# Optimization experiments

Measured on AMD Instinct MI355X. Metric: run time of the kernel, lower is better.

## Reference

```python
import jax, jax.numpy as jnp
import numpy as np

B, J, O = 32, 20, 20
D, H, F, L = 256, 8, 1024, 6
S = J * O
DH = D // H
NL = L + 1  # 6 encoder blocks + final block stacked together


def setup_inputs() -> dict:
    ks = jax.random.split(jax.random.key(0), 16)
    s = 0.02
    am = jax.random.randint(ks[4], (B, J), 0, 2) == 1
    am = am.at[:, 0].set(False)  # at least one unmasked job per row (avoid all -inf softmax)
    return {
        "operations": jax.random.normal(ks[0], (B, J, O, 2), jnp.float32),
        "job_ops_mask": jax.random.normal(ks[1], (B, J, O, O), jnp.float32),
        "ops_machines_mask": jax.random.normal(ks[2], (B, S, S), jnp.float32),
        "jobs_next_op_idx": jax.random.randint(ks[3], (B, J, 1), 0, O),
        "action_mask": am,
        "qkv_w": jax.random.normal(ks[5], (NL, 3 * D, D), jnp.float32) * s,
        "qkv_b": jnp.zeros((NL, 3 * D), jnp.float32),
        "out_w": jax.random.normal(ks[6], (NL, D, D), jnp.float32) * s,
        "out_b": jnp.zeros((NL, D), jnp.float32),
        "ln1_g": jnp.ones((NL, D), jnp.float32),
        "ln1_b": jnp.zeros((NL, D), jnp.float32),
        "ln2_g": jnp.ones((NL, D), jnp.float32),
        "ln2_b": jnp.zeros((NL, D), jnp.float32),
        "ff1_w": jax.random.normal(ks[7], (NL, F, D), jnp.float32) * s,
        "ff1_b": jnp.zeros((NL, F), jnp.float32),
        "ff2_w": jax.random.normal(ks[8], (NL, D, F), jnp.float32) * s,
        "ff2_b": jnp.zeros((NL, D), jnp.float32),
        "op_emb_w": jax.random.normal(ks[9], (D, 2), jnp.float32) * s,
        "op_emb_b": jnp.zeros((D,), jnp.float32),
        "pol_w": jax.random.normal(ks[10], (1, D), jnp.float32) * s,
        "pol_b": jnp.zeros((1,), jnp.float32),
    }


def _ln(x, g, b):
    m = x.mean(-1, keepdims=True)
    v = ((x - m) ** 2).mean(-1, keepdims=True)
    return (x - m) * jax.lax.rsqrt(v + 1e-5) * g + b


def _mha(x, mask, qw, qb, ow, ob):
    N, Sq, _ = x.shape
    qkv = x @ qw.T + qb
    q, k, v = jnp.split(qkv, 3, axis=-1)
    q = q.reshape(N, Sq, H, DH).transpose(0, 2, 1, 3)
    k = k.reshape(N, Sq, H, DH).transpose(0, 2, 1, 3)
    v = v.reshape(N, Sq, H, DH).transpose(0, 2, 1, 3)
    sc = jnp.einsum("nhqd,nhkd->nhqk", q, k) / jnp.sqrt(jnp.float32(DH))
    sc = sc + mask  # additive float attn mask, broadcast over heads where needed
    a = jax.nn.softmax(sc, axis=-1)
    o = jnp.einsum("nhqk,nhkd->nhqd", a, v).transpose(0, 2, 1, 3).reshape(N, Sq, D)
    return o @ ow.T + ob


def _forward(operations, job_ops_mask, ops_machines_mask, jobs_next_op_idx, action_mask,
             qkv_w, qkv_b, out_w, out_b, ln1_g, ln1_b, ln2_g, ln2_b,
             ff1_w, ff1_b, ff2_w, ff2_b, op_emb_w, op_emb_b, pol_w, pol_b):
    def block(x, mask, i):  # pre-norm TransformerEncoderLayer, gelu, dropout=0
        h = _ln(x, ln1_g[i], ln1_b[i])
        x = x + _mha(h, mask, qkv_w[i], qkv_b[i], out_w[i], out_b[i])
        h = _ln(x, ln2_g[i], ln2_b[i])
        ff = jax.nn.gelu(h @ ff1_w[i].T + ff1_b[i], approximate=False) @ ff2_w[i].T + ff2_b[i]
        return x + ff

    # sinusoidal positional encoding over the operation index
    pos = jnp.arange(O, dtype=jnp.float32)[:, None]
    div = jnp.exp(jnp.arange(0, D, 2, dtype=jnp.float32) * (-np.log(10000.0) / D))
    pe = jnp.stack([jnp.sin(pos * div), jnp.cos(pos * div)], axis=-1).reshape(O, D)
    x = operations @ op_emb_w.T + op_emb_b + pe[None, None]  # (B,J,O,D)

    # ALiBi slopes: 1/x^(i+1), x = 256^(1/H)
    base = (2.0 ** 8) ** (1.0 / H)
    slope = (1.0 / base ** jnp.arange(1, H + 1, dtype=jnp.float32))[None, :, None, None]
    job_mask = job_ops_mask.reshape(B * J, 1, O, O) * slope  # (B*J, H, O, O)
    mach_mask = ops_machines_mask[:, None, :, :]  # (B, 1, S, S), identical across heads

    for i in range(L):
        if i % 2 == 0:  # per-job attention over operations
            x = block(x.reshape(B * J, O, D), job_mask, i).reshape(B, J, O, D)
        else:  # per-machine attention over all operations
            x = block(x.reshape(B, S, D), mach_mask, i).reshape(B, J, O, D)

    idx = jnp.broadcast_to(jobs_next_op_idx[:, :, :, None], (B, J, 1, D))
    nxt = jnp.take_along_axis(x, idx, axis=2)[:, :, 0, :]  # (B, J, D)
    kp = jnp.where(action_mask, -jnp.inf, 0.0)[:, None, None, :]  # key padding mask
    nxt = block(nxt, kp, L)
    logits = (nxt @ pol_w.T + pol_b)[:, :, 0]
    return jnp.where(action_mask, -jnp.inf, logits)


def reference(operations, job_ops_mask, ops_machines_mask, jobs_next_op_idx, action_mask,
              qkv_w, qkv_b, out_w, out_b, ln1_g, ln1_b, ln2_g, ln2_b,
              ff1_w, ff1_b, ff2_w, ff2_b, op_emb_w, op_emb_b, pol_w, pol_b):
    return _forward(operations, job_ops_mask, ops_machines_mask, jobs_next_op_idx, action_mask,
                    qkv_w, qkv_b, out_w, out_b, ln1_g, ln1_b, ln2_g, ln2_b,
                    ff1_w, ff1_b, ff2_w, ff2_b, op_emb_w, op_emb_b, pol_w, pol_b)
```

## Files before the change

kernel.cpp:

```cpp
#include <hip/hip_runtime.h>
#include <math.h>

#define B_  32
#define J_  20
#define O_  20
#define S_  400
#define D_  256
#define H_  8
#define F_  1024
#define L_  6
#define T_  12800
#define T2_ 640

#define NEG_BIG (-1e30f)

typedef __attribute__((ext_vector_type(8))) short short8;
typedef __attribute__((ext_vector_type(4))) float f32x4;

__device__ __forceinline__ short f2b(float f) {
  union { float f; unsigned u; } c; c.f = f;
  unsigned r = (c.u + 0x7FFFu + ((c.u >> 16) & 1u)) >> 16;
  return (short)r;
}
__device__ __forceinline__ float b2f(short s) {
  union { unsigned u; float f; } c;
  c.u = ((unsigned)(unsigned short)s) << 16;
  return c.f;
}
__device__ __forceinline__ unsigned addpk(unsigned a, unsigned b) {
  union { unsigned u; float f; } x, y;
  x.u = a << 16;        y.u = b << 16;        float lo = x.f + y.f;
  x.u = a & 0xffff0000u; y.u = b & 0xffff0000u; float hi = x.f + y.f;
  return (unsigned)(unsigned short)f2b(lo) | ((unsigned)(unsigned short)f2b(hi) << 16);
}
__device__ __forceinline__ void async_copy16(const short* g, short* l) {
  __builtin_amdgcn_global_load_lds(
      (const __attribute__((address_space(1))) void*)g,
      (__attribute__((address_space(3))) void*)l, 16, 0, 0);
}

__global__ __launch_bounds__(256) void k_f2b4(
    const float* __restrict__ s0, short* __restrict__ d0,
    const float* __restrict__ s1, short* __restrict__ d1,
    const float* __restrict__ s2, short* __restrict__ d2,
    const float* __restrict__ s3, short* __restrict__ d3)
{
  int bid = blockIdx.x;
  const float* src; short* dst; int base;
  if (bid < 672)        { src = s0; dst = d0; base = bid; }
  else if (bid < 896)   { src = s1; dst = d1; base = bid - 672; }
  else if (bid < 1792)  { src = s2; dst = d2; base = bid - 896; }
  else                  { src = s3; dst = d3; base = bid - 1792; }
  int i = (base * 256 + threadIdx.x) * 8;
  float4 a = *(const float4*)(src + i);
  float4 b = *(const float4*)(src + i + 4);
  short8 o;
  o[0] = f2b(a.x); o[1] = f2b(a.y); o[2] = f2b(a.z); o[3] = f2b(a.w);
  o[4] = f2b(b.x); o[5] = f2b(b.y); o[6] = f2b(b.z); o[7] = f2b(b.w);
  *(short8*)(dst + i) = o;
}

__global__ __launch_bounds__(640) void k_maskconv(
    const void* __restrict__ am_raw, int* __restrict__ am_out)
{
  __shared__ int isInt32;
  const int tid = threadIdx.x;
  if (tid == 0) isInt32 = 1;
  __syncthreads();
  if (tid < 160) {
    int v = ((const int*)am_raw)[tid];
    if (v != 0 && v != 1) atomicAnd(&isInt32, 0);
  }
  __syncthreads();
  if (tid < 640) {
    int v;
    if (isInt32) v = ((const int*)am_raw)[tid] != 0;
    else         v = ((const unsigned char*)am_raw)[tid] != 0;
    am_out[tid] = v;
  }
}

__global__ __launch_bounds__(256) void k_embed(
    const float* __restrict__ ops, const float* __restrict__ ew,
    const float* __restrict__ eb, short* __restrict__ x)
{
  int idx = blockIdx.x * 256 + threadIdx.x;
  int d = idx & 255;
  int t = idx >> 8;
  int o = t % O_;
  float a0 = ops[(size_t)t * 2 + 0], a1 = ops[(size_t)t * 2 + 1];
  int k = d >> 1;
  float div = expf((float)(2 * k) * -0.03597789207803197f);
  float ang = (float)o * div;
  float pe = (d & 1) ? cosf(ang) : sinf(ang);
  x[idx] = f2b(a0 * ew[d * 2 + 0] + a1 * ew[d * 2 + 1] + eb[d] + pe);
}

__global__ __launch_bounds__(256) void k_ln(
    const short* __restrict__ x, const float* __restrict__ g, const float* __restrict__ b,
    short* __restrict__ out, int nTok)
{
  int gid = blockIdx.x * 256 + threadIdx.x;
  int tok = gid >> 6, lane = threadIdx.x & 63;
  if (tok >= nTok) return;
  int2 pk = ((const int2*)(x + (size_t)tok * 256))[lane];
  union { unsigned u; float f; } c;
  float vx, vy, vz, vw;
  c.u = (unsigned)pk.x << 16;        vx = c.f;
  c.u = (unsigned)pk.x & 0xffff0000u; vy = c.f;
  c.u = (unsigned)pk.y << 16;        vz = c.f;
  c.u = (unsigned)pk.y & 0xffff0000u; vw = c.f;
  float s = vx + vy + vz + vw;
  #pragma unroll
  for (int off = 32; off > 0; off >>= 1) s += __shfl_down(s, off);
  float mean = __shfl(s, 0) * (1.f / 256.f);
  float dx = vx - mean, dy = vy - mean, dz = vz - mean, dw = vw - mean;
  float q = dx * dx + dy * dy + dz * dz + dw * dw;
  #pragma unroll
  for (int off = 32; off > 0; off >>= 1) q += __shfl_down(q, off);
  float var = __shfl(q, 0) * (1.f / 256.f);
  float inv = 1.f / sqrtf(var + 1e-5f);
  float4 gv = ((const float4*)g)[lane];
  float4 bv = ((const float4*)b)[lane];
  float ox = dx * inv * gv.x + bv.x;
  float oy = dy * inv * gv.y + bv.y;
  float oz = dz * inv * gv.z + bv.z;
  float ow = dw * inv * gv.w + bv.w;
  int2 po;
  po.x = (int)(unsigned short)f2b(ox) | ((int)(unsigned short)f2b(oy) << 16);
  po.y = (int)(unsigned short)f2b(oz) | ((int)(unsigned short)f2b(ow) << 16);
  ((int2*)(out + (size_t)tok * 256))[lane] = po;
}

__global__ __launch_bounds__(256) void k_gemm_bf16(
    const short* __restrict__ A, const short* __restrict__ W,
    const float* __restrict__ bias, const short* __restrict__ R,
    short* __restrict__ C, int M, int N, int K, int act)
{
  __shared__ short LDS_[17408];
  short* Asf = LDS_;
  short* Bsf = LDS_ + 8192;
  short* Csf = LDS_;
  const int tid  = threadIdx.x;
  const int lane = tid & 63;
  const int wv   = tid >> 6;
  const int lm   = lane & 15;
  const int quad = lane >> 4;
  const int wm   = (wv >> 1) * 64;
  const int wn   = (wv & 1) * 64;
  const int n0 = blockIdx.x * 128;
  const int m0 = blockIdx.y * 128;

  f32x4 acc[4][4] = {};

  for (int k0 = 0; k0 < K; k0 += 64) {
    __syncthreads();
    #pragma unroll
    for (int i = 0; i < 4; ++i) {
      const int c    = tid + 256 * i;
      const int row  = c >> 3;
      const int kc8  = ((c & 7) ^ (row & 7)) * 8;
      async_copy16(A + (size_t)(m0 + row) * K + k0 + kc8, &Asf[c * 8]);
      async_copy16(W + (size_t)(n0 + row) * K + k0 + kc8, &Bsf[c * 8]);
    }
    __syncthreads();
    #pragma unroll
    for (int kh = 0; kh < 2; ++kh) {
      short8 af[4], bf[4];
      #pragma unroll
      for (int i = 0; i < 4; ++i) {
        const int row  = wm + i * 16 + lm;
        const int slot = (kh * 4 + quad) ^ (lm & 7);
        af[i] = *(short8*)&Asf[(row * 8 + slot) * 8];
      }
      #pragma unroll
      for (int j = 0; j < 4; ++j) {
        const int row  = wn + j * 16 + lm;
        const int slot = (kh * 4 + quad) ^ (lm & 7);
        bf[j] = *(short8*)&Bsf[(row * 8 + slot) * 8];
      }
      #pragma unroll
      for (int i = 0; i < 4; ++i)
        #pragma unroll
        for (int j = 0; j < 4; ++j)
          acc[i][j] = __builtin_amdgcn_mfma_f32_16x16x32_bf16(af[i], bf[j], acc[i][j], 0, 0, 0);
    }
  }

  __syncthreads();
  #pragma unroll
  for (int j = 0; j < 4; ++j) {
    const int ccol = wn + j * 16 + lm;
    const float bv = bias[n0 + ccol];
    #pragma unroll
    for (int i = 0; i < 4; ++i) {
      #pragma unroll
      for (int r = 0; r < 4; ++r) {
        const int row = wm + i * 16 + quad * 4 + r;
        float vvv = acc[i][j][r] + bv;
        if (act) vvv = vvv / (1.f + __expf(-1.702f * vvv));
        Csf[row * 136 + ccol] = f2b(vvv);
      }
    }
  }
  __syncthreads();
  {
    const int srow = tid >> 1, sh = (tid & 1) * 64;
    const size_t gbase = (size_t)(m0 + srow) * N + n0 + sh;
    const short* ls = &Csf[srow * 136 + sh];
    #pragma unroll
    for (int u = 0; u < 8; ++u) {
      uint4 v = *(const uint4*)(ls + u * 8);
      if (R) {
        uint4 rv = *(const uint4*)(R + gbase + u * 8);
        v.x = addpk(v.x, rv.x); v.y = addpk(v.y, rv.y);
        v.z = addpk(v.z, rv.z); v.w = addpk(v.w, rv.w);
      }
      *(uint4*)(C + gbase + u * 8) = v;
    }
  }
}

__global__ __launch_bounds__(256) void k_gemm_ln(
    const short* __restrict__ A, const short* __restrict__ W,
    const float* __restrict__ bias, const short* __restrict__ R,
    short* __restrict__ X, short* __restrict__ Hout,
    const float* __restrict__ g, const float* __restrict__ bb_,
    int M, int K)
{
  __shared__ short LDS_[4096 + 16896];
  short* Asf = LDS_;
  short* Bsf = LDS_ + 4096;
  short* Csf = LDS_ + 4096;
  const int tid  = threadIdx.x;
  const int lane = tid & 63;
  const int wv   = tid >> 6;
  const int lm   = lane & 15;
  const int quad = lane >> 4;
  const int wn   = wv * 64;
  const int m0   = blockIdx.x * 64;

  f32x4 acc[4][4] = {};

  for (int k0 = 0; k0 < K; k0 += 64) {
    __syncthreads();
    #pragma unroll
    for (int i = 0; i < 2; ++i) {
      const int c   = tid + 256 * i;
      const int row = c >> 3;
      const int kc8 = ((c & 7) ^ (row & 7)) * 8;
      async_copy16(A + (size_t)(m0 + row) * K + k0 + kc8, &Asf[c * 8]);
    }
    #pragma unroll
    for (int i = 0; i < 8; ++i) {
      const int c   = tid + 256 * i;
      const int row = c >> 3;
      const int kc8 = ((c & 7) ^ (row & 7)) * 8;
      async_copy16(W + (size_t)row * K + k0 + kc8, &Bsf[c * 8]);
    }
    __syncthreads();
    #pragma unroll
    for (int kh = 0; kh < 2; ++kh) {
      short8 af[4], bf[4];
      #pragma unroll
      for (int i = 0; i < 4; ++i) {
        const int row  = i * 16 + lm;
        const int slot = (kh * 4 + quad) ^ (lm & 7);
        af[i] = *(short8*)&Asf[(row * 8 + slot) * 8];
      }
      #pragma unroll
      for (int j = 0; j < 4; ++j) {
        const int row  = wn + j * 16 + lm;
        const int slot = (kh * 4 + quad) ^ (lm & 7);
        bf[j] = *(short8*)&Bsf[(row * 8 + slot) * 8];
      }
      #pragma unroll
      for (int i = 0; i < 4; ++i)
        #pragma unroll
        for (int j = 0; j < 4; ++j)
          acc[i][j] = __builtin_amdgcn_mfma_f32_16x16x32_bf16(af[i], bf[j], acc[i][j], 0, 0, 0);
    }
  }

  __syncthreads();
  #pragma unroll
  for (int j = 0; j < 4; ++j) {
    const int ccol = wn + j * 16 + lm;
    const float bv = bias[ccol];
    #pragma unroll
    for (int i = 0; i < 4; ++i) {
      #pragma unroll
      for (int r = 0; r < 4; ++r) {
        const int row = i * 16 + quad * 4 + r;
        Csf[row * 264 + ccol] = f2b(acc[i][j][r] + bv);
      }
    }
  }
  __syncthreads();

  {
    const int row = tid >> 2, cb = (tid & 3) * 64;
    const size_t gbase = (size_t)(m0 + row) * 256 + cb;
    const short* ls = &Csf[row * 264 + cb];
    uint4 xv[8];
    float s1 = 0.f, s2 = 0.f;
    #pragma unroll
    for (int u = 0; u < 8; ++u) {
      uint4 v = *(const uint4*)(ls + u * 8);
      uint4 rv = *(const uint4*)(R + gbase + u * 8);
      v.x = addpk(v.x, rv.x); v.y = addpk(v.y, rv.y);
      v.z = addpk(v.z, rv.z); v.w = addpk(v.w, rv.w);
      xv[u] = v;
      *(uint4*)(X + gbase + u * 8) = v;
      #pragma unroll
      for (int w2 = 0; w2 < 4; ++w2) {
        unsigned pv = (&v.x)[w2];
        union { unsigned u; float f; } c1, c2;
        c1.u = pv << 16; c2.u = pv & 0xffff0000u;
        s1 += c1.f + c2.f;
        s2 += c1.f * c1.f + c2.f * c2.f;
      }
    }
    s1 += __shfl_xor(s1, 1); s2 += __shfl_xor(s2, 1);
    s1 += __shfl_xor(s1, 2); s2 += __shfl_xor(s2, 2);
    const float mean = s1 * (1.f / 256.f);
    const float var  = s2 * (1.f / 256.f) - mean * mean;
    const float inv  = 1.f / sqrtf(var + 1e-5f);
    #pragma unroll
    for (int u = 0; u < 8; ++u) {
      float4 g0 = *(const float4*)(g + cb + u * 8);
      float4 g1 = *(const float4*)(g + cb + u * 8 + 4);
      float4 b0 = *(const float4*)(bb_ + cb + u * 8);
      float4 b1 = *(const float4*)(bb_ + cb + u * 8 + 4);
      auto lnpk = [&](unsigned pv, float ga, float gb2, float ba, float bb2) -> unsigned {
        union { unsigned u; float f; } c1, c2;
        c1.u = pv << 16; c2.u = pv & 0xffff0000u;
        float lo = (c1.f - mean) * inv * ga + ba;
        float hi = (c2.f - mean) * inv * gb2 + bb2;
        return (unsigned)(unsigned short)f2b(lo) | ((unsigned)(unsigned short)f2b(hi) << 16);
      };
      uint4 hv;
      hv.x = lnpk(xv[u].x, g0.x, g0.y, b0.x, b0.y);
      hv.y = lnpk(xv[u].y, g0.z, g0.w, b0.z, b0.w);
      hv.z = lnpk(xv[u].z, g1.x, g1.y, b1.x, b1.y);
      hv.w = lnpk(xv[u].w, g1.z, g1.w, b1.z, b1.w);
      *(uint4*)(Hout + gbase + u * 8) = hv;
    }
  }
}

#define QSTR 776
#define PSTR20 40
__global__ __launch_bounds__(512) void k_attn20_mfma(
    const short* __restrict__ qkv, short* __restrict__ att,
    const float* __restrict__ jmask, const int* __restrict__ amask, int mode)
{
  __shared__ short QK[32 * QSTR];
  __shared__ short Ps[8][32 * PSTR20];
  const int seq  = blockIdx.x;
  const int tid  = threadIdx.x;
  const int wv   = tid >> 6;
  const int lane = tid & 63;
  const int l15  = lane & 15;
  const int quad = lane >> 4;
  const float scale = 0.1767766952966369f;

  for (int e = tid; e < 3072; e += 512) {
    int row = e / 96, c8 = (e % 96) * 8;
    uint4 v = {0u, 0u, 0u, 0u};
    if (row < 20) v = *(const uint4*)(qkv + ((size_t)seq * 20 + row) * 768 + c8);
    *(uint4*)&QK[row * QSTR + c8] = v;
  }
  __syncthreads();

  const short8 aq0 = *(short8*)&QK[(0  + l15) * QSTR + wv * 32 + quad * 8];
  const short8 aq1 = *(short8*)&QK[(16 + l15) * QSTR + wv * 32 + quad * 8];
  const short8 bk0 = *(short8*)&QK[(0  + l15) * QSTR + 256 + wv * 32 + quad * 8];
  const short8 bk1 = *(short8*)&QK[(16 + l15) * QSTR + 256 + wv * 32 + quad * 8];
  f32x4 z4 = {0.f, 0.f, 0.f, 0.f};
  f32x4 s00 = __builtin_amdgcn_mfma_f32_16x16x32_bf16(aq0, bk0, z4, 0, 0, 0);
  f32x4 s01 = __builtin_amdgcn_mfma_f32_16x16x32_bf16(aq0, bk1, z4, 0, 0, 0);
  f32x4 s10 = __builtin_amdgcn_mfma_f32_16x16x32_bf16(aq1, bk0, z4, 0, 0, 0);
  f32x4 s11 = __builtin_amdgcn_mfma_f32_16x16x32_bf16(aq1, bk1, z4, 0, 0, 0);

  const float slope = exp2f(-(float)(wv + 1));
  short* psw = &Ps[wv][0];
  float l0[4] = {0.f, 0.f, 0.f, 0.f};
  float l1[4] = {0.f, 0.f, 0.f, 0.f};

  #pragma unroll
  for (int kt = 0; kt < 2; ++kt) {
    const int k  = kt * 16 + l15;
    const int kc = (k < 20) ? k : 19;
    float madd1 = 0.f;
    if (mode == 1) madd1 = amask[seq * 20 + kc] ? NEG_BIG : 0.f;
    #pragma unroll
    for (int qt = 0; qt < 2; ++qt) {
      f32x4 s = (kt == 0) ? (qt == 0 ? s00 : s10) : (qt == 0 ? s01 : s11);
      #pragma unroll
      for (int r = 0; r < 4; ++r) {
        const int q  = qt * 16 + quad * 4 + r;
        const int qc = (q < 20) ? q : 19;
        float sv = s[r] * scale;
        if (mode == 0) sv += jmask[(size_t)seq * 400 + qc * 20 + kc] * slope;
        else           sv += madd1;
        float p = (k < 20) ? __expf(fminf(sv, 40.f)) : 0.f;
        if (qt == 0) l0[r] += p; else l1[r] += p;
        psw[q * PSTR20 + k] = f2b(p);
      }
    }
  }
  #pragma unroll
  for (int r = 0; r < 4; ++r) {
    float t0 = l0[r];
    t0 += __shfl_xor(t0, 1); t0 += __shfl_xor(t0, 2);
    t0 += __shfl_xor(t0, 4); t0 += __shfl_xor(t0, 8);
    l0[r] = 1.f / t0;
    float t1 = l1[r];
    t1 += __shfl_xor(t1, 1); t1 += __shfl_xor(t1, 2);
    t1 += __shfl_xor(t1, 4); t1 += __shfl_xor(t1, 8);
    l1[r] = 1.f / t1;
  }

  const short8 pf0 = *(short8*)&psw[(0  + l15) * PSTR20 + quad * 8];
  const short8 pf1 = *(short8*)&psw[(16 + l15) * PSTR20 + quad * 8];
  #pragma unroll
  for (int dt = 0; dt < 2; ++dt) {
    const int d = wv * 32 + dt * 16 + l15;
    short8 vf;
    #pragma unroll
    for (int j = 0; j < 8; ++j)
      vf[j] = QK[(quad * 8 + j) * QSTR + 512 + d];
    f32x4 o0 = __builtin_amdgcn_mfma_f32_16x16x32_bf16(pf0, vf, z4, 0, 0, 0);
    f32x4 o1 = __builtin_amdgcn_mfma_f32_16x16x32_bf16(pf1, vf, z4, 0, 0, 0);
    #pragma unroll
    for (int r = 0; r < 4; ++r) {
      const int q = quad * 4 + r;
      att[((size_t)seq * 20 + q) * 256 + d] = f2b(o0[r] * l0[r]);
    }
    if (quad == 0) {
      #pragma unroll
      for (int r = 0; r < 4; ++r) {
        const int q = 16 + r;
        att[((size_t)seq * 20 + q) * 256 + d] = f2b(o1[r] * l1[r]);
      }
    }
  }
}

#define VSTR 36
#define PSTRW 40
__global__ __launch_bounds__(512) void k_attn400_mfma(
    const short* __restrict__ qkv, short* __restrict__ att,
    const float* __restrict__ mmask)
{
  __shared__ short Wl[8 * 1792];

  const int id   = blockIdx.x;
  const int b    = (id >> 3) / 25 * 8 + (id & 7);
  const int qt   = (id >> 3) % 25;
  const int tid  = threadIdx.x;
  const int wv   = tid >> 6;
  const int lane = tid & 63;
  const int l15  = lane & 15;
  const int quad = lane >> 4;
  const int q0   = qt * 16;
  const float scale = 0.1767766952966369f;

  short* Vw = &Wl[wv * 1792];
  short* Pw = &Wl[wv * 1792 + 1152];
  const short* qbase = qkv + (size_t)b * 400 * 768;

  const short8 af = *(const short8*)(qbase + (size_t)(q0 + l15) * 768 + wv * 32 + quad * 8);

  f32x4 accO[2] = {};
  float lsum = 0.f;
  const float* mrow = mmask + ((size_t)b * 400 + q0 + l15) * 400;

  const int vrow = lane >> 1;
  const int vch  = (lane & 1) * 2;
  const int vdst = vrow * VSTR + vch * 8;

  short8 kf0, kf1;
  float4 mA4, mB4;
  auto prefKM = [&](int k0) {
    kf0 = *(const short8*)(qbase + (size_t)(k0 + l15) * 768 + 256 + wv * 32 + quad * 8);
    int kr = k0 + 16 + l15; if (kr > 399) kr = 399;
    kf1 = *(const short8*)(qbase + (size_t)kr * 768 + 256 + wv * 32 + quad * 8);
    mA4 = *(const float4*)(mrow + k0 + quad * 4);
    int kb = k0 + 16 + quad * 4; if (kb > 396) kb = 396;
    mB4 = *(const float4*)(mrow + kb);
  };
  prefKM(0);

  for (int k0 = 0; k0 < 416; k0 += 32) {
    int vr = k0 + vrow; if (vr > 399) vr = 399;
    const short* vp = qbase + (size_t)vr * 768 + 512 + wv * 32 + vch * 8;
    const uint4 v0 = *(const uint4*)vp;
    const uint4 v1 = *(const uint4*)(vp + 8);

    const short8 ck0 = kf0, ck1 = kf1;
    const float4 cA = mA4, cB = mB4;

    f32x4 z4 = {0.f, 0.f, 0.f, 0.f};
    f32x4 s0 = __builtin_amdgcn_mfma_f32_16x16x32_bf16(ck0, af, z4, 0, 0, 0);
    f32x4 s1 = __builtin_amdgcn_mfma_f32_16x16x32_bf16(ck1, af, z4, 0, 0, 0);

    if (k0 + 32 < 416) prefKM(k0 + 32);

    float p0[4], p1[4];
    #pragma unroll
    for (int r = 0; r < 4; ++r) {
      const int kB = k0 + 16 + quad * 4 + r;
      float svA = s0[r] * scale + (&cA.x)[r];
      float svB = (kB < 400) ? (s1[r] * scale + (&cB.x)[r]) : NEG_BIG;
      p0[r] = __expf(fminf(svA, 40.f));
      p1[r] = __expf(fminf(svB, 40.f));
      lsum += p0[r] + p1[r];
    }

    unsigned pk00, pk01, pk10, pk11;
    asm("v_cvt_pk_bf16_f32 %0, %1, %2" : "=v"(pk00) : "v"(p0[0]), "v"(p0[1]));
    asm("v_cvt_pk_bf16_f32 %0, %1, %2" : "=v"(pk01) : "v"(p0[2]), "v"(p0[3]));
    asm("v_cvt_pk_bf16_f32 %0, %1, %2" : "=v"(pk10) : "v"(p1[0]), "v"(p1[1]));
    asm("v_cvt_pk_bf16_f32 %0, %1, %2" : "=v"(pk11) : "v"(p1[2]), "v"(p1[3]));
    uint2 w0; w0.x = pk00; w0.y = pk01;
    uint2 w1; w1.x = pk10; w1.y = pk11;
    *(uint2*)&Pw[l15 * PSTRW + quad * 4]      = w0;
    *(uint2*)&Pw[l15 * PSTRW + 16 + quad * 4] = w1;
    const short8 pf = *(short8*)&Pw[l15 * PSTRW + quad * 8];

    *(uint4*)&Vw[vdst]     = v0;
    *(uint4*)&Vw[vdst + 8] = v1;
    #pragma unroll
    for (int c = 0; c < 2; ++c) {
      short8 vf;
      #pragma unroll
      for (int j = 0; j < 8; ++j)
        vf[j] = Vw[(quad * 8 + j) * VSTR + c * 16 + l15];
      accO[c] = __builtin_amdgcn_mfma_f32_16x16x32_bf16(vf, pf, accO[c], 0, 0, 0);
    }
  }

  lsum += __shfl_xor(lsum, 16);
  lsum += __shfl_xor(lsum, 32);
  const float inv = 1.f / lsum;

  #pragma unroll
  for (int c = 0; c < 2; ++c) {
    float a0 = accO[c][0] * inv, a1 = accO[c][1] * inv;
    float a2 = accO[c][2] * inv, a3 = accO[c][3] * inv;
    unsigned o01, o23;
    asm("v_cvt_pk_bf16_f32 %0, %1, %2" : "=v"(o01) : "v"(a0), "v"(a1));
    asm("v_cvt_pk_bf16_f32 %0, %1, %2" : "=v"(o23) : "v"(a2), "v"(a3));
    uint2 ov; ov.x = o01; ov.y = o23;
    *(uint2*)&att[((size_t)b * 400 + q0 + l15) * 256 + wv * 32 + c * 16 + quad * 4] = ov;
  }
}

__global__ __launch_bounds__(256) void k_gather2(
    const short* __restrict__ x, const short* __restrict__ h,
    const int* __restrict__ idx, short* __restrict__ x2, short* __restrict__ h2)
{
  int t = blockIdx.x * 256 + threadIdx.x;
  if (t >= 640 * 16) return;
  int bj = t >> 4, c = t & 15;
  int o = idx[bj];
  size_t src = ((size_t)bj * 20 + o) * 256;
  ((uint4*)(x2 + (size_t)bj * 256))[c] = ((const uint4*)(x + src))[c];
  ((uint4*)(h2 + (size_t)bj * 256))[c] = ((const uint4*)(h + src))[c];
}

__global__ __launch_bounds__(256) void k_logits(
    const short* __restrict__ x2, const float* __restrict__ pw, const float* __restrict__ pb,
    const int* __restrict__ am, float* __restrict__ out)
{
  int gid = blockIdx.x * 256 + threadIdx.x;
  int row = gid >> 6, lane = threadIdx.x & 63;
  int2 pk = ((const int2*)(x2 + (size_t)row * 256))[lane];
  union { unsigned u; float f; } c;
  float vx, vy, vz, vw;
  c.u = (unsigned)pk.x << 16;         vx = c.f;
  c.u = (unsigned)pk.x & 0xffff0000u; vy = c.f;
  c.u = (unsigned)pk.y << 16;         vz = c.f;
  c.u = (unsigned)pk.y & 0xffff0000u; vw = c.f;
  float4 w = ((const float4*)pw)[lane];
  float s = vx * w.x + vy * w.y + vz * w.z + vw * w.w;
  #pragma unroll
  for (int off = 32; off > 0; off >>= 1) s += __shfl_down(s, off);
  if (lane == 0) out[row] = am[row] ? NEG_BIG : (s + pb[0]);
}

extern "C" void kernel_launch(void* const* d_in, const int* in_sizes, int n_in,
                              void* d_out, int out_size, void* d_ws, size_t ws_size,
                              hipStream_t stream)
{
  (void)in_sizes; (void)n_in; (void)out_size; (void)ws_size;
  const float* operations        = (const float*)d_in[0];
  const float* job_ops_mask      = (const float*)d_in[1];
  const float* ops_machines_mask = (const float*)d_in[2];
  const int*   jobs_next_op_idx  = (const int*)d_in[3];
  const void*  action_mask_raw   = (const void*)d_in[4];
  const float* qkv_w = (const float*)d_in[5];
  const float* qkv_b = (const float*)d_in[6];
  const float* out_w = (const float*)d_in[7];
  const float* out_b = (const float*)d_in[8];
  const float* ln1_g = (const float*)d_in[9];
  const float* ln1_b = (const float*)d_in[10];
  const float* ln2_g = (const float*)d_in[11];
  const float* ln2_b = (const float*)d_in[12];
  const float* ff1_w = (const float*)d_in[13];
  const float* ff1_b = (const float*)d_in[14];
  const float* ff2_w = (const float*)d_in[15];
  const float* ff2_b = (const float*)d_in[16];
  const float* op_emb_w = (const float*)d_in[17];
  const float* op_emb_b = (const float*)d_in[18];
  const float* pol_w = (const float*)d_in[19];
  const float* pol_b = (const float*)d_in[20];
  float* out = (float*)d_out;

  short* x    = (short*)d_ws;
  short* x2   = x + (size_t)T_ * D_;
  short* h    = x2 + (size_t)T2_ * D_;
  short* big  = h + (size_t)T_ * D_;
  short* h2   = big + (size_t)T_ * F_;
  short* big2 = h2 + (size_t)T2_ * D_;
  int*   amc  = (int*)(big2 + (size_t)T2_ * F_);
  short* bwq  = (short*)(amc + 640);
  short* bwo  = bwq + (size_t)7 * 768 * 256;
  short* bwf1 = bwo + (size_t)7 * 256 * 256;
  short* bwf2 = bwf1 + (size_t)7 * 1024 * 256;

  auto gemm = [&](const short* A, const short* Wb, const float* bias, const short* R,
                  short* C, int M, int N, int K, int act) {
    k_gemm_bf16<<<dim3(N / 128, M / 128), dim3(256), 0, stream>>>(
        A, Wb, bias, R, C, M, N, K, act);
  };
  auto gemm_ln = [&](const short* A, const short* Wb, const float* bias, const short* R,
                     short* X, short* Hout, const float* g, const float* b, int M, int K) {
    k_gemm_ln<<<dim3(M / 64), dim3(256), 0, stream>>>(
        A, Wb, bias, R, X, Hout, g, b, M, K);
  };

  k_f2b4<<<dim3(2688), 256, 0, stream>>>(qkv_w, bwq, out_w, bwo, ff1_w, bwf1, ff2_w, bwf2);
  k_maskconv<<<dim3(1), dim3(640), 0, stream>>>(action_mask_raw, amc);
  k_embed<<<dim3(T_ * D_ / 256), dim3(256), 0, stream>>>(operations, op_emb_w, op_emb_b, x);
  k_ln<<<dim3(T_ / 4), 256, 0, stream>>>(x, ln1_g, ln1_b, h, T_);

  for (int i = 0; i < L_; ++i) {
    const short* qw  = bwq  + (size_t)i * 768 * 256;
    const float* qb  = qkv_b + (size_t)i * 768;
    const short* ow  = bwo  + (size_t)i * 256 * 256;
    const float* ob  = out_b + (size_t)i * 256;
    const short* f1w = bwf1 + (size_t)i * 1024 * 256;
    const float* f1b = ff1_b + (size_t)i * 1024;
    const short* f2w = bwf2 + (size_t)i * 256 * 1024;
    const float* f2b_ = ff2_b + (size_t)i * 256;
    gemm(h, qw, qb, nullptr, big, T_, 768, 256, 0);
    if ((i & 1) == 0)
      k_attn20_mfma<<<dim3(640), 512, 0, stream>>>(big, h, job_ops_mask, nullptr, 0);
    else
      k_attn400_mfma<<<dim3(800), 512, 0, stream>>>(big, h, ops_machines_mask);
    gemm_ln(h, ow, ob, x, x, h, ln2_g + i * D_, ln2_b + i * D_, T_, 256);
    gemm(h, f1w, f1b, nullptr, big, T_, 1024, 256, 1);
    gemm_ln(big, f2w, f2b_, x, x, h, ln1_g + (i + 1) * D_, ln1_b + (i + 1) * D_, T_, 1024);
  }

  k_gather2<<<dim3(40), 256, 0, stream>>>(x, h, jobs_next_op_idx, x2, h2);

  {
    int i = L_;
    const short* qw  = bwq  + (size_t)i * 768 * 256;
    const float* qb  = qkv_b + (size_t)i * 768;
    const short* ow  = bwo  + (size_t)i * 256 * 256;
    const float* ob  = out_b + (size_t)i * 256;
    const short* f1w = bwf1 + (size_t)i * 1024 * 256;
    const float* f1b = ff1_b + (size_t)i * 1024;
    const short* f2w = bwf2 + (size_t)i * 256 * 1024;
    const float* f2b_ = ff2_b + (size_t)i * 256;
    gemm(h2, qw, qb, nullptr, big2, T2_, 768, 256, 0);
    k_attn20_mfma<<<dim3(32), 512, 0, stream>>>(big2, h2, nullptr, amc, 1);
    gemm_ln(h2, ow, ob, x2, x2, h2, ln2_g + i * D_, ln2_b + i * D_, T2_, 256);
    gemm(h2, f1w, f1b, nullptr, big2, T2_, 1024, 256, 1);
    gemm(big2, f2w, f2b_, x2, x2, T2_, 256, 1024, 0);
  }

  k_logits<<<dim3(160), 256, 0, stream>>>(x2, pol_w, pol_b, amc, out);
}
```

Before: 982.8 us.

## Convert machine mask to bf16 once and stage per-tile mask rows in LDS

The 400x400 machine attention mask is converted to bf16 once per call in the weight-conversion kernel (2500 extra blocks), so each of the three machine-attention layers reads half the bytes. Each attention block cooperatively loads its 16 mask rows into shared memory, removing per-wave redundant global float4 mask loads (8 waves read the same rows). V loads are also prefetched one iteration ahead and written to LDS earlier. Trade-offs: the mask is rounded to bf16, which changes precision, and there is an extra conversion pass plus extra LDS use.

```diff
diff --git a/kernel.cpp b/kernel.cpp
--- a/kernel.cpp
+++ b/kernel.cpp
@@ -43,14 +43,16 @@
     const float* __restrict__ s0, short* __restrict__ d0,
     const float* __restrict__ s1, short* __restrict__ d1,
     const float* __restrict__ s2, short* __restrict__ d2,
-    const float* __restrict__ s3, short* __restrict__ d3)
+    const float* __restrict__ s3, short* __restrict__ d3,
+    const float* __restrict__ s4, short* __restrict__ d4)
 {
   int bid = blockIdx.x;
   const float* src; short* dst; int base;
   if (bid < 672)        { src = s0; dst = d0; base = bid; }
   else if (bid < 896)   { src = s1; dst = d1; base = bid - 672; }
   else if (bid < 1792)  { src = s2; dst = d2; base = bid - 896; }
-  else                  { src = s3; dst = d3; base = bid - 1792; }
+  else if (bid < 2688)  { src = s3; dst = d3; base = bid - 1792; }
+  else                  { src = s4; dst = d4; base = bid - 2688; }
   int i = (base * 256 + threadIdx.x) * 8;
   float4 a = *(const float4*)(src + i);
   float4 b = *(const float4*)(src + i + 4);
@@ -450,11 +452,13 @@
 
 #define VSTR 36
 #define PSTRW 40
+#define MSTR 424
 __global__ __launch_bounds__(512) void k_attn400_mfma(
     const short* __restrict__ qkv, short* __restrict__ att,
-    const float* __restrict__ mmask)
+    const short* __restrict__ mbf)
 {
   __shared__ short Wl[8 * 1792];
+  __shared__ short Ml[16 * MSTR];
 
   const int id   = blockIdx.x;
   const int b    = (id >> 3) / 25 * 8 + (id & 7);
@@ -467,6 +471,14 @@
   const int q0   = qt * 16;
   const float scale = 0.1767766952966369f;
 
+  for (int e = tid; e < 16 * 52; e += 512) {
+    const int row = e / 52, cc = e % 52;
+    uint4 v = {0u, 0u, 0u, 0u};
+    if (cc < 50)
+      v = *(const uint4*)(mbf + ((size_t)(b * 400 + q0 + row)) * 400 + cc * 8);
+    *(uint4*)&Ml[row * MSTR + cc * 8] = v;
+  }
+
   short* Vw = &Wl[wv * 1792];
   short* Pw = &Wl[wv * 1792 + 1152];
   const short* qbase = qkv + (size_t)b * 400 * 768;
@@ -475,45 +487,65 @@
 
   f32x4 accO[2] = {};
   float lsum = 0.f;
-  const float* mrow = mmask + ((size_t)b * 400 + q0 + l15) * 400;
 
   const int vrow = lane >> 1;
   const int vch  = (lane & 1) * 2;
   const int vdst = vrow * VSTR + vch * 8;
 
   short8 kf0, kf1;
-  float4 mA4, mB4;
-  auto prefKM = [&](int k0) {
+  uint4  nv0, nv1;
+  auto prefK = [&](int k0) {
     kf0 = *(const short8*)(qbase + (size_t)(k0 + l15) * 768 + 256 + wv * 32 + quad * 8);
     int kr = k0 + 16 + l15; if (kr > 399) kr = 399;
     kf1 = *(const short8*)(qbase + (size_t)kr * 768 + 256 + wv * 32 + quad * 8);
-    mA4 = *(const float4*)(mrow + k0 + quad * 4);
-    int kb = k0 + 16 + quad * 4; if (kb > 396) kb = 396;
-    mB4 = *(const float4*)(mrow + kb);
   };
-  prefKM(0);
-
-  for (int k0 = 0; k0 < 416; k0 += 32) {
+  auto prefV = [&](int k0) {
     int vr = k0 + vrow; if (vr > 399) vr = 399;
     const short* vp = qbase + (size_t)vr * 768 + 512 + wv * 32 + vch * 8;
-    const uint4 v0 = *(const uint4*)vp;
-    const uint4 v1 = *(const uint4*)(vp + 8);
-
+    nv0 = *(const uint4*)vp;
+    nv1 = *(const uint4*)(vp + 8);
+  };
+  prefK(0);
+  prefV(0);
+
+  __syncthreads();
+
+  const short* mrow = &Ml[l15 * MSTR];
+
+  for (int k0 = 0; k0 < 416; k0 += 32) {
+    const uint4 v0 = nv0, v1 = nv1;
     const short8 ck0 = kf0, ck1 = kf1;
-    const float4 cA = mA4, cB = mB4;
+
+    *(uint4*)&Vw[vdst]     = v0;
+    *(uint4*)&Vw[vdst + 8] = v1;
 
     f32x4 z4 = {0.f, 0.f, 0.f, 0.f};
     f32x4 s0 = __builtin_amdgcn_mfma_f32_16x16x32_bf16(ck0, af, z4, 0, 0, 0);
     f32x4 s1 = __builtin_amdgcn_mfma_f32_16x16x32_bf16(ck1, af, z4, 0, 0, 0);
 
-    if (k0 + 32 < 416) prefKM(k0 + 32);
+    if (k0 + 32 < 416) { prefK(k0 + 32); prefV(k0 + 32); }
+
+    uint2 ma = *(const uint2*)(mrow + k0 + quad * 4);
+    uint2 mb = *(const uint2*)(mrow + k0 + 16 + quad * 4);
+    float mAv[4], mBv[4];
+    {
+      union { unsigned u; float f; } c;
+      c.u = ma.x << 16;         mAv[0] = c.f;
+      c.u = ma.x & 0xffff0000u; mAv[1] = c.f;
+      c.u = ma.y << 16;         mAv[2] = c.f;
+      c.u = ma.y & 0xffff0000u; mAv[3] = c.f;
+      c.u = mb.x << 16;         mBv[0] = c.f;
+      c.u = mb.x & 0xffff0000u; mBv[1] = c.f;
+      c.u = mb.y << 16;         mBv[2] = c.f;
+      c.u = mb.y & 0xffff0000u; mBv[3] = c.f;
+    }
 
     float p0[4], p1[4];
     #pragma unroll
     for (int r = 0; r < 4; ++r) {
       const int kB = k0 + 16 + quad * 4 + r;
-      float svA = s0[r] * scale + (&cA.x)[r];
-      float svB = (kB < 400) ? (s1[r] * scale + (&cB.x)[r]) : NEG_BIG;
+      float svA = s0[r] * scale + mAv[r];
+      float svB = (kB < 400) ? (s1[r] * scale + mBv[r]) : NEG_BIG;
       p0[r] = __expf(fminf(svA, 40.f));
       p1[r] = __expf(fminf(svB, 40.f));
       lsum += p0[r] + p1[r];
@@ -530,8 +562,6 @@
     *(uint2*)&Pw[l15 * PSTRW + 16 + quad * 4] = w1;
     const short8 pf = *(short8*)&Pw[l15 * PSTRW + quad * 8];
 
-    *(uint4*)&Vw[vdst]     = v0;
-    *(uint4*)&Vw[vdst + 8] = v1;
     #pragma unroll
     for (int c = 0; c < 2; ++c) {
       short8 vf;
@@ -630,6 +660,7 @@
   short* bwo  = bwq + (size_t)7 * 768 * 256;
   short* bwf1 = bwo + (size_t)7 * 256 * 256;
   short* bwf2 = bwf1 + (size_t)7 * 1024 * 256;
+  short* mbf  = bwf2 + (size_t)7 * 256 * 1024;
 
   auto gemm = [&](const short* A, const short* Wb, const float* bias, const short* R,
                   short* C, int M, int N, int K, int act) {
@@ -642,7 +673,8 @@
         A, Wb, bias, R, X, Hout, g, b, M, K);
   };
 
-  k_f2b4<<<dim3(2688), 256, 0, stream>>>(qkv_w, bwq, out_w, bwo, ff1_w, bwf1, ff2_w, bwf2);
+  k_f2b4<<<dim3(5188), 256, 0, stream>>>(qkv_w, bwq, out_w, bwo, ff1_w, bwf1,
+                                         ff2_w, bwf2, ops_machines_mask, mbf);
   k_maskconv<<<dim3(1), dim3(640), 0, stream>>>(action_mask_raw, amc);
   k_embed<<<dim3(T_ * D_ / 256), dim3(256), 0, stream>>>(operations, op_emb_w, op_emb_b, x);
   k_ln<<<dim3(T_ / 4), 256, 0, stream>>>(x, ln1_g, ln1_b, h, T_);
@@ -660,7 +692,7 @@
     if ((i & 1) == 0)
       k_attn20_mfma<<<dim3(640), 512, 0, stream>>>(big, h, job_ops_mask, nullptr, 0);
     else
-      k_attn400_mfma<<<dim3(800), 512, 0, stream>>>(big, h, ops_machines_mask);
+      k_attn400_mfma<<<dim3(800), 512, 0, stream>>>(big, h, mbf);
     gemm_ln(h, ow, ob, x, x, h, ln2_g + i * D_, ln2_b + i * D_, T_, 256);
     gemm(h, f1w, f1b, nullptr, big, T_, 1024, 256, 1);
     gemm_ln(big, f2w, f2b_, x, x, h, ln1_g + (i + 1) * D_, ln1_b + (i + 1) * D_, T_, 1024);
```

Result: no change. 974.1 us (-0.9%).
